# Kernel tuning notes

Hardware: AMD Instinct MI355X
Metric: run time of the kernel (lower is better)

## Reference

```python
import jax, jax.numpy as jnp
import numpy as np

N_HEAD = 16

def setup_inputs() -> dict:
    key = jax.random.key(0)
    ks = jax.random.split(key, 9)
    B, T, C = 2, 2048, 1024
    s = 0.02
    return {
        "x": jax.random.normal(ks[0], (B, T, C), dtype=jnp.float32),
        "Wk": jax.random.normal(ks[1], (C, C), dtype=jnp.float32) * s,
        "bk": jnp.zeros((C,), dtype=jnp.float32),
        "Wq": jax.random.normal(ks[2], (C, C), dtype=jnp.float32) * s,
        "bq": jnp.zeros((C,), dtype=jnp.float32),
        "Wv": jax.random.normal(ks[3], (C, C), dtype=jnp.float32) * s,
        "bv": jnp.zeros((C,), dtype=jnp.float32),
        "Wp": jax.random.normal(ks[4], (C, C), dtype=jnp.float32) * s,
        "bp": jnp.zeros((C,), dtype=jnp.float32),
    }

def reference(x, Wk, bk, Wq, bq, Wv, bv, Wp, bp):
    B, T, C = x.shape
    H = N_HEAD
    D = C // H
    # projections -> [B, H, T, D]
    def split_heads(y):
        return y.reshape(B, T, H, D).transpose(0, 2, 1, 3)
    k = split_heads(x @ Wk.T + bk)
    q = split_heads(x @ Wq.T + bq)
    v = split_heads(x @ Wv.T + bv)
    scale = 1.0 / jnp.sqrt(jnp.asarray(D, dtype=x.dtype))
    att = jnp.einsum("bhtd,bhsd->bhts", q, k) * scale  # [B,H,T,T]
    causal = jnp.tril(jnp.ones((T, T), dtype=bool))
    att = jnp.where(causal, att, jnp.asarray(-jnp.inf, dtype=att.dtype))
    att = jax.nn.softmax(att, axis=-1)
    y = jnp.einsum("bhts,bhsd->bhtd", att, v)  # [B,H,T,D]
    y = y.transpose(0, 2, 1, 3).reshape(B, T, C)
    return y @ Wp.T + bp
```

## Files before the change

### kernel.cpp

```cpp
#include <hip/hip_runtime.h>
#include <stdint.h>

typedef unsigned short u16;
typedef __attribute__((ext_vector_type(8))) short short8;
typedef __attribute__((ext_vector_type(4))) short short4v;
typedef __attribute__((ext_vector_type(4))) float float4v;

#define NB 2
#define NT 2048
#define NC 1024
#define NH 16
#define ND 64
#define NM (NB*NT)

#if defined(__has_builtin)
#if __has_builtin(__builtin_amdgcn_mfma_f32_16x16x16bf16_1k)
#define MFMA16(a, b, c) __builtin_amdgcn_mfma_f32_16x16x16bf16_1k(a, b, c, 0, 0, 0)
#endif
#endif
#ifndef MFMA16
static __device__ __forceinline__ float4v mfma16_asm(short4v a, short4v b, float4v c) {
  asm volatile("v_mfma_f32_16x16x16_bf16 %0, %1, %2, %0" : "+v"(c) : "v"(a), "v"(b));
  return c;
}
#define MFMA16(a, b, c) mfma16_asm(a, b, c)
#endif

#if defined(__has_builtin)
#if __has_builtin(__builtin_amdgcn_exp2f)
#define EXP2(x) __builtin_amdgcn_exp2f(x)
#endif
#endif
#ifndef EXP2
extern "C" __device__ float __ocml_native_exp2_f32(float);
#define EXP2(x) __ocml_native_exp2_f32(x)
#endif

#define WB4 asm volatile("s_waitcnt vmcnt(4)\n\ts_barrier" ::: "memory")
#define WB3 asm volatile("s_waitcnt vmcnt(3)\n\ts_barrier" ::: "memory")
#define WB0 asm volatile("s_waitcnt vmcnt(0)\n\ts_barrier" ::: "memory")
#define BAR_PLAIN asm volatile("s_barrier" ::: "memory")

__device__ __forceinline__ u16 f2bf(float f) {
  union { float f; uint32_t u; } v; v.f = f;
  uint32_t u = v.u;
  u += 0x7fffu + ((u >> 16) & 1u);
  return (u16)(u >> 16);
}
__device__ __forceinline__ float bf2f(u16 u) {
  union { uint32_t u; float f; } v; v.u = ((uint32_t)u) << 16; return v.f;
}

__device__ __forceinline__ short4v pack4bf(float a, float b, float c, float d) {
  union { uint32_t u[2]; short4v s; } r;
  r.u[0] = __builtin_amdgcn_perm(__float_as_uint(b), __float_as_uint(a), 0x07060302u);
  r.u[1] = __builtin_amdgcn_perm(__float_as_uint(d), __float_as_uint(c), 0x07060302u);
  return r.s;
}

__device__ __forceinline__ void gld_lds16(const u16* g, u16* lds) {
  __builtin_amdgcn_global_load_lds(
      (const __attribute__((address_space(1))) uint32_t*)g,
      (__attribute__((address_space(3))) uint32_t*)lds,
      16, 0, 0);
}

__global__ __launch_bounds__(256) void cast_all(
    const float* __restrict__ x,  const float* __restrict__ wk,
    const float* __restrict__ wq, const float* __restrict__ wv,
    const float* __restrict__ wp,
    u16* __restrict__ xb, u16* __restrict__ wkb, u16* __restrict__ wqb,
    u16* __restrict__ wvb, u16* __restrict__ wpb) {
  const int NX = NM * NC / 4;
  const int NW = NC * NC / 4;
  int i = blockIdx.x * 256 + threadIdx.x;
  const float* src; u16* dst; int off;
  if (i < NX)            { src = x;  dst = xb;  off = i; }
  else if (i < NX+NW)    { src = wk; dst = wkb; off = i - NX; }
  else if (i < NX+2*NW)  { src = wq; dst = wqb; off = i - NX - NW; }
  else if (i < NX+3*NW)  { src = wv; dst = wvb; off = i - NX - 2*NW; }
  else if (i < NX+4*NW)  { src = wp; dst = wpb; off = i - NX - 3*NW; }
  else return;
  float4v f = ((const float4v*)src)[off];
  short4v o;
  o.x = (short)f2bf(f.x); o.y = (short)f2bf(f.y);
  o.z = (short)f2bf(f.z); o.w = (short)f2bf(f.w);
  ((short4v*)dst)[off] = o;
}

__global__ __launch_bounds__(256, 4) void qkv_gemm(
    const u16* __restrict__ xb,
    const u16* __restrict__ wqb, const u16* __restrict__ wkb, const u16* __restrict__ wvb,
    const float* __restrict__ bq, const float* __restrict__ bk, const float* __restrict__ bv,
    u16* __restrict__ Q, u16* __restrict__ K, u16* __restrict__ Vt) {
  __shared__ u16 S[4][128 * 32];
  const int id  = blockIdx.x;
  const int x8  = id & 7;
  const int rr  = id >> 3;
  const int mti = rr & 31;
  const int mat = rr >> 5;
  const int n0  = x8 * 128;
  const int m0  = mti * 128;
  const u16*   W    = (mat == 0) ? wqb : (mat == 1) ? wkb : wvb;
  const float* bias = (mat == 0) ? bq  : (mat == 1) ? bk  : bv;

  const int tid = threadIdx.x, wave = tid >> 6, lane = tid & 63;
  const int quad = lane >> 4, l15 = lane & 15;
  const int wm = wave >> 1, wn = wave & 1;

  const u16* A_tile = xb + (size_t)m0 * NC;
  const u16* W_tile = W  + (size_t)n0 * NC;

  const int srow = wave * 16 + (lane >> 2);
  const int sgc  = (lane & 3) ^ (srow & 3);
  const int soff = srow * NC + sgc * 8;
  const int ldsb0 = wave * 16 * 32;
  const int ldsb1 = (64 + wave * 16) * 32;

  float4v acc[4][4];
#pragma unroll
  for (int i = 0; i < 4; i++)
#pragma unroll
    for (int j = 0; j < 4; j++) acc[i][j] = (float4v){0.f, 0.f, 0.f, 0.f};

  auto stage = [&](int ki, int p) {
    const u16* a = A_tile + ki * 32;
    const u16* w = W_tile + ki * 32;
    gld_lds16(a + soff,           S[p]     + ldsb0);
    gld_lds16(a + 64 * NC + soff, S[p]     + ldsb1);
    gld_lds16(w + soff,           S[2 + p] + ldsb0);
    gld_lds16(w + 64 * NC + soff, S[2 + p] + ldsb1);
  };

  stage(0, 0);
  for (int ki = 0; ki < 32; ki++) {
    const int p = ki & 1;
    if (ki < 31) { stage(ki + 1, p ^ 1); WB4; } else { WB0; }
    const u16* As = S[p];
    const u16* Bs = S[2 + p];
    short8 af[4], bf[4];
#pragma unroll
    for (int mt = 0; mt < 4; mt++) {
      int row = wm * 64 + mt * 16 + l15;
      int e   = quad ^ (row & 3);
      af[mt] = *(const short8*)(As + row * 32 + e * 8);
    }
#pragma unroll
    for (int nt = 0; nt < 4; nt++) {
      int row = wn * 64 + nt * 16 + l15;
      int e   = quad ^ (row & 3);
      bf[nt] = *(const short8*)(Bs + row * 32 + e * 8);
    }
#pragma unroll
    for (int mt = 0; mt < 4; mt++)
#pragma unroll
      for (int nt = 0; nt < 4; nt++)
        acc[mt][nt] = __builtin_amdgcn_mfma_f32_16x16x32_bf16(af[mt], bf[nt], acc[mt][nt], 0, 0, 0);
    if (ki < 31) BAR_PLAIN;
  }

  if (mat != 2) {
    u16* dst = (mat == 0) ? Q : K;
    const float osc = (mat == 0) ? 0.18033688f : 1.0f;
#pragma unroll
    for (int nt = 0; nt < 4; nt++) {
      int col = n0 + wn * 64 + nt * 16 + l15;
      float bval = bias[col];
#pragma unroll
      for (int mt = 0; mt < 4; mt++) {
        int rowb = m0 + wm * 64 + mt * 16 + quad * 4;
#pragma unroll
        for (int r = 0; r < 4; r++)
          dst[(size_t)(rowb + r) * NC + col] = f2bf((acc[mt][nt][r] + bval) * osc);
      }
    }
  } else {
    BAR_PLAIN;
    u16* tile = (u16*)S;
#pragma unroll
    for (int nt = 0; nt < 4; nt++) {
      int c = wn * 64 + nt * 16 + l15;
      float bval = bias[n0 + c];
#pragma unroll
      for (int mt = 0; mt < 4; mt++) {
#pragma unroll
        for (int r = 0; r < 4; r++) {
          int mr  = mt * 4 + r;
          int off = wm * 64 + quad * 16 + mr;
          int ck  = (off >> 3) ^ (c & 15);
          tile[c * 128 + ck * 8 + (off & 7)] = f2bf(acc[mt][nt][r] + bval);
        }
      }
    }
    __syncthreads();
    const int b  = m0 >> 11, t0 = m0 & 2047;
    const int bh0 = b * NH + (n0 >> 6);
#pragma unroll
    for (int it = 0; it < 8; it++) {
      int idx = it * 256 + tid;
      int c = idx >> 4, ck = idx & 15;
      short8 v = *(const short8*)(tile + c * 128 + ((ck ^ (c & 15)) * 8));
      *(short8*)(Vt + ((size_t)(bh0 + (c >> 6)) * ND + (c & 63)) * NT + t0 + ck * 8) = v;
    }
  }
}

__global__ __launch_bounds__(256, 4) void attn(
    const u16* __restrict__ Q, const u16* __restrict__ K,
    const u16* __restrict__ Vt, u16* __restrict__ O,
    u16* __restrict__ Opart, float* __restrict__ Lpart) {
  __shared__ u16 Kc[2][64 * 64];
  __shared__ u16 Vc[2][64 * 64];

  const int tid = threadIdx.x, wave = tid >> 6, lane = tid & 63;
  const int quad = lane >> 4, l15 = lane & 15;
  const int c8 = lane & 7, r8 = lane >> 3;
  const int id = blockIdx.x;
  const int gq = (id >> 3) & 31;
  const int gp = id >> 8;
  static const uint8_t QT[8][4] = {
      {15, 16, 4, 0}, {30, 31, 3, 1}, {13, 14, 9, 2}, {25, 26, 10, 5},
      {27, 28, 17, 6}, {29, 11, 18, 7}, {12, 20, 22, 8}, {23, 24, 19, 21}};
  const int cls = QT[gq >> 2][((gq & 3) + gp) & 3];
  const int bh = (id & 7) + 8 * gp;
  const int b = bh >> 4, h = bh & 15;

  int tile, k, c_lo, c_hi, sbase;
  if (cls < 5)        { tile = cls;
                        c_lo = 0; c_hi = 2 * tile + 1; sbase = -1; }
  else if (cls < 17)  { tile = 5 + ((cls - 5) >> 1); k = (cls - 5) & 1;
                        int half = tile + 1;
                        c_lo = k * half; c_hi = c_lo + half - 1;
                        sbase = (tile - 5) * 2 + k; }
  else                { int d3 = cls - 17; int t3 = d3 / 3; k = d3 - 3 * t3;
                        tile = 11 + t3; int C = 2 * tile + 2;
                        c_lo = (k * C) / 3; c_hi = ((k + 1) * C) / 3 - 1;
                        sbase = 12 + t3 * 3 + k; }
  const bool partial = (sbase >= 0);
  const int qb0 = tile * 128 + wave * 32;

  short8 qf[2][2];
#pragma unroll
  for (int j = 0; j < 2; j++) {
    const u16* qrow = Q + (size_t)(b * NT + qb0 + j * 16 + l15) * NC + h * ND + quad * 8;
    qf[j][0] = *(const short8*)(qrow);
    qf[j][1] = *(const short8*)(qrow + 32);
  }

  const short4v vone = {(short)0x3F80, (short)0x3F80, (short)0x3F80, (short)0x3F80};
  float4v l_acc[2];
  float4v o_acc[2][4];
#pragma unroll
  for (int j = 0; j < 2; j++) {
    l_acc[j] = (float4v){0.f, 0.f, 0.f, 0.f};
#pragma unroll
    for (int dt = 0; dt < 4; dt++) o_acc[j][dt] = (float4v){0.f, 0.f, 0.f, 0.f};
  }

  int kOff[2], vOff[2], ldsOff[2];
#pragma unroll
  for (int ii = 0; ii < 2; ii++) {
    int row = wave * 16 + ii * 8 + r8;
    int gc  = c8 ^ (row & 7);
    kOff[ii]   = row * NC + gc * 8;
    vOff[ii]   = row * NT + gc * 8;
    ldsOff[ii] = (wave * 16 + ii * 8) * 64;
  }
  const u16* Kbase = K  + (size_t)b * NT * NC + h * ND;
  const u16* Vbase = Vt + (size_t)bh * ND * NT;

  auto stage = [&](int ci) {
    const int p = (ci - c_lo) & 1;
    const u16* kc = Kbase + (size_t)ci * (64 * NC);
    const u16* vc = Vbase + ci * 64;
#pragma unroll
    for (int ii = 0; ii < 2; ii++) {
      gld_lds16(kc + kOff[ii], Kc[p] + ldsOff[ii]);
      gld_lds16(vc + vOff[ii], Vc[p] + ldsOff[ii]);
    }
  };

  stage(c_lo);
  for (int i = c_lo; i <= c_hi; i++) {
    const int p = (i - c_lo) & 1;
    if (i < c_hi) { stage(i + 1); WB4; } else { WB0; }
    const u16* Ks = Kc[p];
    const u16* Vs = Vc[p];

    short4v pf[2][4];
#pragma unroll
    for (int sub = 0; sub < 4; sub++) {
      float4v a0 = (float4v){0.f, 0.f, 0.f, 0.f};
      float4v a1 = (float4v){0.f, 0.f, 0.f, 0.f};
#pragma unroll
      for (int kk = 0; kk < 2; kk++) {
        int row = sub * 16 + l15;
        int ch  = (kk * 4 + quad) ^ (row & 7);
        short8 kf = *(const short8*)(Ks + row * 64 + ch * 8);
        a0 = __builtin_amdgcn_mfma_f32_16x16x32_bf16(kf, qf[0][kk], a0, 0, 0, 0);
        a1 = __builtin_amdgcn_mfma_f32_16x16x32_bf16(kf, qf[1][kk], a1, 0, 0, 0);
      }
#pragma unroll
      for (int j = 0; j < 2; j++) {
        const float4v& a = (j == 0) ? a0 : a1;
        const bool mj = (i * 64 + 63) > (qb0 + j * 16);
        const int qg = qb0 + j * 16 + l15;
        float pv[4];
#pragma unroll
        for (int r = 0; r < 4; r++) {
          float pp = EXP2(a[r]);
          if (mj) {
            int sg = i * 64 + sub * 16 + quad * 4 + r;
            if (sg > qg) pp = 0.f;
          }
          pv[r] = pp;
        }
        pf[j][sub] = pack4bf(pv[0], pv[1], pv[2], pv[3]);
      }
    }

#pragma unroll
    for (int j = 0; j < 2; j++) {
      l_acc[j] = MFMA16(vone, pf[j][0], l_acc[j]);
      l_acc[j] = MFMA16(vone, pf[j][1], l_acc[j]);
      l_acc[j] = MFMA16(vone, pf[j][2], l_acc[j]);
      l_acc[j] = MFMA16(vone, pf[j][3], l_acc[j]);
    }

#pragma unroll
    for (int dt = 0; dt < 4; dt++) {
      int row = dt * 16 + l15;
      int swz = row & 7;
      short8 vA = *(const short8*)(Vs + row * 64 + ((2 * quad)     ^ swz) * 8);
      short8 vB = *(const short8*)(Vs + row * 64 + ((2 * quad + 1) ^ swz) * 8);
      short4v vA0 = __builtin_shufflevector(vA, vA, 0, 1, 2, 3);
      short4v vA1 = __builtin_shufflevector(vA, vA, 4, 5, 6, 7);
      short4v vB0 = __builtin_shufflevector(vB, vB, 0, 1, 2, 3);
      short4v vB1 = __builtin_shufflevector(vB, vB, 4, 5, 6, 7);
#pragma unroll
      for (int j = 0; j < 2; j++) {
        o_acc[j][dt] = MFMA16(vA0, pf[j][0], o_acc[j][dt]);
        o_acc[j][dt] = MFMA16(vA1, pf[j][1], o_acc[j][dt]);
        o_acc[j][dt] = MFMA16(vB0, pf[j][2], o_acc[j][dt]);
        o_acc[j][dt] = MFMA16(vB1, pf[j][3], o_acc[j][dt]);
      }
    }
    if (i < c_hi) BAR_PLAIN;
  }

  float l_tot[2] = {l_acc[0][0], l_acc[1][0]};

  if (!partial) {
#pragma unroll
    for (int j = 0; j < 2; j++) {
      float inv_l = 1.f / l_tot[j];
      const size_t orow = (size_t)(b * NT + qb0 + j * 16 + l15) * NC + h * ND;
#pragma unroll
      for (int dt = 0; dt < 4; dt++)
        *(short4v*)(O + orow + dt * 16 + quad * 4) =
            pack4bf(o_acc[j][dt][0] * inv_l, o_acc[j][dt][1] * inv_l,
                    o_acc[j][dt][2] * inv_l, o_acc[j][dt][3] * inv_l);
    }
  } else {
    const int slab = bh * 27 + sbase;
    u16* ob = Opart + (size_t)slab * 8192;
#pragma unroll
    for (int j = 0; j < 2; j++) {
      const int row = wave * 32 + j * 16 + l15;
#pragma unroll
      for (int dt = 0; dt < 4; dt++)
        *(short4v*)(ob + row * 64 + dt * 16 + quad * 4) =
            pack4bf(o_acc[j][dt][0], o_acc[j][dt][1],
                    o_acc[j][dt][2], o_acc[j][dt][3]);
      if (quad == 0)
        Lpart[slab * 128 + row] = l_tot[j];
    }
  }
}

__global__ __launch_bounds__(256) void combine(
    const u16* __restrict__ Opart, const float* __restrict__ Lp, u16* __restrict__ O) {
  int idx  = blockIdx.x * 256 + threadIdx.x;
  int tIdx = idx >> 10;
  int rem8 = idx & 1023;
  int row  = rem8 >> 3, d0 = (rem8 & 7) * 8;
  int bh   = tIdx / 11;
  int tt   = tIdx - bh * 11;
  int tile = 5 + tt;
  int S, sb;
  if (tile < 11) { S = 2; sb = (tile - 5) * 2; }
  else           { S = 3; sb = 12 + (tile - 11) * 3; }
  int slab0 = bh * 27 + sb;
  float osum[8] = {0.f, 0.f, 0.f, 0.f, 0.f, 0.f, 0.f, 0.f};
  float lsum = 0.f;
  for (int s = 0; s < S; s++) {
    short8 v = *(const short8*)(Opart + (size_t)(slab0 + s) * 8192 + rem8 * 8);
#pragma unroll
    for (int e = 0; e < 8; e++) osum[e] += bf2f((u16)v[e]);
    lsum += Lp[(slab0 + s) * 128 + row];
  }
  float inv = 1.f / lsum;
  short8 o;
#pragma unroll
  for (int e = 0; e < 8; e++) o[e] = (short)f2bf(osum[e] * inv);
  int b = bh >> 4, h = bh & 15;
  int t = tile * 128 + row;
  *(short8*)(O + (size_t)(b * NT + t) * NC + h * ND + d0) = o;
}

__global__ __launch_bounds__(256, 5) void out_gemm(
    const u16* __restrict__ Ob, const u16* __restrict__ wpb,
    const float* __restrict__ bp, float* __restrict__ out) {
  __shared__ u16 Sa[2][64 * 32];
  __shared__ u16 Sb[2][128 * 32];
  const int n0 = blockIdx.x * 128;
  const int m0 = blockIdx.y * 64;
  const int tid = threadIdx.x, wave = tid >> 6, lane = tid & 63;
  const int quad = lane >> 4, l15 = lane & 15;
  const int wm = wave >> 1, wn = wave & 1;

  const u16* A_tile = Ob  + (size_t)m0 * NC;
  const u16* W_tile = wpb + (size_t)n0 * NC;
  const int srow = wave * 16 + (lane >> 2);
  const int sgc  = (lane & 3) ^ (srow & 3);
  const int soff = srow * NC + sgc * 8;
  const int ldsb0 = wave * 16 * 32;
  const int ldsb1 = (64 + wave * 16) * 32;

  float4v acc[2][4];
#pragma unroll
  for (int i = 0; i < 2; i++)
#pragma unroll
    for (int j = 0; j < 4; j++) acc[i][j] = (float4v){0.f, 0.f, 0.f, 0.f};

  auto stage = [&](int ki, int p) {
    const u16* a = A_tile + ki * 32;
    const u16* w = W_tile + ki * 32;
    gld_lds16(a + soff,           Sa[p] + ldsb0);
    gld_lds16(w + soff,           Sb[p] + ldsb0);
    gld_lds16(w + 64 * NC + soff, Sb[p] + ldsb1);
  };

  stage(0, 0);
  for (int ki = 0; ki < 32; ki++) {
    const int p = ki & 1;
    if (ki < 31) { stage(ki + 1, p ^ 1); WB3; } else { WB0; }
    short8 af[2], bf[4];
#pragma unroll
    for (int mt = 0; mt < 2; mt++) {
      int row = wm * 32 + mt * 16 + l15;
      int e   = quad ^ (row & 3);
      af[mt] = *(const short8*)(Sa[p] + row * 32 + e * 8);
    }
#pragma unroll
    for (int nt = 0; nt < 4; nt++) {
      int row = wn * 64 + nt * 16 + l15;
      int e   = quad ^ (row & 3);
      bf[nt] = *(const short8*)(Sb[p] + row * 32 + e * 8);
    }
#pragma unroll
    for (int mt = 0; mt < 2; mt++)
#pragma unroll
      for (int nt = 0; nt < 4; nt++)
        acc[mt][nt] = __builtin_amdgcn_mfma_f32_16x16x32_bf16(af[mt], bf[nt], acc[mt][nt], 0, 0, 0);
    if (ki < 31) BAR_PLAIN;
  }

#pragma unroll
  for (int nt = 0; nt < 4; nt++) {
    int col = n0 + wn * 64 + nt * 16 + l15;
    float bval = bp[col];
#pragma unroll
    for (int mt = 0; mt < 2; mt++) {
      int rowb = m0 + wm * 32 + mt * 16 + quad * 4;
#pragma unroll
      for (int r = 0; r < 4; r++)
        out[(rowb + r) * NC + col] = acc[mt][nt][r] + bval;
    }
  }
}

extern "C" void kernel_launch(void* const* d_in, const int* in_sizes, int n_in,
                              void* d_out, int out_size, void* d_ws, size_t ws_size,
                              hipStream_t stream) {
  const float* x  = (const float*)d_in[0];
  const float* Wk = (const float*)d_in[1];
  const float* bk = (const float*)d_in[2];
  const float* Wq = (const float*)d_in[3];
  const float* bq = (const float*)d_in[4];
  const float* Wv = (const float*)d_in[5];
  const float* bv = (const float*)d_in[6];
  const float* Wp = (const float*)d_in[7];
  const float* bp = (const float*)d_in[8];
  float* out = (float*)d_out;

  uint8_t* ws = (uint8_t*)d_ws;
  const size_t MB = 1u << 20;
  u16* xb    = (u16*)(ws + 0 * MB);
  u16* wkb   = (u16*)(ws + 8 * MB);
  u16* wqb   = (u16*)(ws + 10 * MB);
  u16* wvb   = (u16*)(ws + 12 * MB);
  u16* wpb   = (u16*)(ws + 14 * MB);
  u16* Qb    = (u16*)(ws + 16 * MB);
  u16* Kb    = (u16*)(ws + 24 * MB);
  u16* Vtb   = (u16*)(ws + 32 * MB);
  u16* Ob    = (u16*)(ws + 40 * MB);
  u16* Opart = (u16*)(ws + 0 * MB);
  float* Lpart = (float*)(ws + 13 * MB + 512 * 1024);

  cast_all<<<8192, 256, 0, stream>>>(x, Wk, Wq, Wv, Wp, xb, wkb, wqb, wvb, wpb);
  qkv_gemm<<<768, 256, 0, stream>>>(xb, wqb, wkb, wvb, bq, bk, bv, Qb, Kb, Vtb);
  attn<<<1024, 256, 0, stream>>>(Qb, Kb, Vtb, Ob, Opart, Lpart);
  combine<<<1408, 256, 0, stream>>>(Opart, Lpart, Ob);
  out_gemm<<<dim3(8, 64), 256, 0, stream>>>(Ob, wpb, bp, out);
}
```

Baseline: 182.8 us.

## Restructure pipeline barriers, remap qkv block order, stage Q/K epilogue through LDS

All three main loops move to a single wait-all-plus-barrier at the top of each iteration, issue the next stage afterwards, and drop the trailing barrier. The aim is to halve the barrier count while the prefetch still overlaps compute. The qkv_gemm block index is remapped so consecutive blocks share N tiles and group M tiles. Its Q/K epilogue now writes through a swizzled LDS tile and stores 16-byte vectors, replacing scattered 2-byte global stores. The attention loop raises wave priority around its MFMA work, and out_gemm occupancy drops from 5 to 4. Waiting on vmcnt(0) before issuing the next loads may expose more memory latency than the previous partial waits.

```diff
diff --git a/kernel.cpp b/kernel.cpp
--- a/kernel.cpp
+++ b/kernel.cpp
@@ -36,8 +36,6 @@
 #define EXP2(x) __ocml_native_exp2_f32(x)
 #endif
 
-#define WB4 asm volatile("s_waitcnt vmcnt(4)\n\ts_barrier" ::: "memory")
-#define WB3 asm volatile("s_waitcnt vmcnt(3)\n\ts_barrier" ::: "memory")
 #define WB0 asm volatile("s_waitcnt vmcnt(0)\n\ts_barrier" ::: "memory")
 #define BAR_PLAIN asm volatile("s_barrier" ::: "memory")
 
@@ -95,10 +93,11 @@
     u16* __restrict__ Q, u16* __restrict__ K, u16* __restrict__ Vt) {
   __shared__ u16 S[4][128 * 32];
   const int id  = blockIdx.x;
-  const int x8  = id & 7;
-  const int rr  = id >> 3;
-  const int mti = rr & 31;
-  const int mat = rr >> 5;
+  const int mg  = id & 7;
+  const int mti = mg * 4 + ((id >> 3) & 3);
+  const int rr  = id >> 5;
+  const int x8  = rr & 7;
+  const int mat = rr >> 3;
   const int n0  = x8 * 128;
   const int m0  = mti * 128;
   const u16*   W    = (mat == 0) ? wqb : (mat == 1) ? wkb : wvb;
@@ -135,7 +134,8 @@
   stage(0, 0);
   for (int ki = 0; ki < 32; ki++) {
     const int p = ki & 1;
-    if (ki < 31) { stage(ki + 1, p ^ 1); WB4; } else { WB0; }
+    WB0;
+    if (ki < 31) stage(ki + 1, p ^ 1);
     const u16* As = S[p];
     const u16* Bs = S[2 + p];
     short8 af[4], bf[4];
@@ -156,23 +156,36 @@
 #pragma unroll
       for (int nt = 0; nt < 4; nt++)
         acc[mt][nt] = __builtin_amdgcn_mfma_f32_16x16x32_bf16(af[mt], bf[nt], acc[mt][nt], 0, 0, 0);
-    if (ki < 31) BAR_PLAIN;
   }
 
   if (mat != 2) {
     u16* dst = (mat == 0) ? Q : K;
     const float osc = (mat == 0) ? 0.18033688f : 1.0f;
+    BAR_PLAIN;
+    u16* tile = (u16*)S;
 #pragma unroll
     for (int nt = 0; nt < 4; nt++) {
-      int col = n0 + wn * 64 + nt * 16 + l15;
-      float bval = bias[col];
+      int col = wn * 64 + nt * 16 + l15;
+      float bval = bias[n0 + col];
 #pragma unroll
       for (int mt = 0; mt < 4; mt++) {
-        int rowb = m0 + wm * 64 + mt * 16 + quad * 4;
-#pragma unroll
-        for (int r = 0; r < 4; r++)
-          dst[(size_t)(rowb + r) * NC + col] = f2bf((acc[mt][nt][r] + bval) * osc);
+        int rowb = wm * 64 + mt * 16 + quad * 4;
+#pragma unroll
+        for (int r = 0; r < 4; r++) {
+          int row = rowb + r;
+          tile[row * 128 + (col ^ (((row >> 2) & 7) << 4))] =
+              f2bf((acc[mt][nt][r] + bval) * osc);
+        }
       }
+    }
+    __syncthreads();
+#pragma unroll
+    for (int it = 0; it < 8; it++) {
+      int idx = it * 256 + tid;
+      int row = idx >> 4, ck = idx & 15;
+      int s = (row >> 2) & 7;
+      short8 v = *(const short8*)(tile + row * 128 + ((((ck >> 1) ^ s) << 4) | ((ck & 1) << 3)));
+      *(short8*)(dst + (size_t)(m0 + row) * NC + n0 + ck * 8) = v;
     }
   } else {
     BAR_PLAIN;
@@ -283,9 +296,11 @@
   stage(c_lo);
   for (int i = c_lo; i <= c_hi; i++) {
     const int p = (i - c_lo) & 1;
-    if (i < c_hi) { stage(i + 1); WB4; } else { WB0; }
+    WB0;
+    if (i < c_hi) stage(i + 1);
     const u16* Ks = Kc[p];
     const u16* Vs = Vc[p];
+    __builtin_amdgcn_s_setprio(1);
 
     short4v pf[2][4];
 #pragma unroll
@@ -345,7 +360,7 @@
         o_acc[j][dt] = MFMA16(vB1, pf[j][3], o_acc[j][dt]);
       }
     }
-    if (i < c_hi) BAR_PLAIN;
+    __builtin_amdgcn_s_setprio(0);
   }
 
   float l_tot[2] = {l_acc[0][0], l_acc[1][0]};
@@ -408,7 +423,7 @@
   *(short8*)(O + (size_t)(b * NT + t) * NC + h * ND + d0) = o;
 }
 
-__global__ __launch_bounds__(256, 5) void out_gemm(
+__global__ __launch_bounds__(256, 4) void out_gemm(
     const u16* __restrict__ Ob, const u16* __restrict__ wpb,
     const float* __restrict__ bp, float* __restrict__ out) {
   __shared__ u16 Sa[2][64 * 32];
@@ -444,7 +459,8 @@
   stage(0, 0);
   for (int ki = 0; ki < 32; ki++) {
     const int p = ki & 1;
-    if (ki < 31) { stage(ki + 1, p ^ 1); WB3; } else { WB0; }
+    WB0;
+    if (ki < 31) stage(ki + 1, p ^ 1);
     short8 af[2], bf[4];
 #pragma unroll
     for (int mt = 0; mt < 2; mt++) {
@@ -463,7 +479,6 @@
 #pragma unroll
       for (int nt = 0; nt < 4; nt++)
         acc[mt][nt] = __builtin_amdgcn_mfma_f32_16x16x32_bf16(af[mt], bf[nt], acc[mt][nt], 0, 0, 0);
-    if (ki < 31) BAR_PLAIN;
   }
 
 #pragma unroll
```

Result: no change. 179.4 us (-1.9%).
